# Kernel optimization log

Hardware: AMD Instinct MI355X
Metric: run time of the kernel (lower is better)

Reference implementation:

```python
import jax, jax.numpy as jnp
import numpy as np
from jax import lax

WIN = 11  # window_size


def _uniform_filter_valid(x, win):
    """Separable uniform (box) filter, VALID padding. x: [B,1,H,W].
    Equivalent to scipy uniform_filter followed by skimage's pad-cropping,
    since cropped positions only use fully-interior windows."""
    kh = jnp.full((1, 1, win, 1), 1.0 / win, dtype=x.dtype)
    kw = jnp.full((1, 1, 1, win), 1.0 / win, dtype=x.dtype)
    dn = ('NCHW', 'OIHW', 'NCHW')
    x = lax.conv_general_dilated(x, kh, (1, 1), 'VALID', dimension_numbers=dn)
    x = lax.conv_general_dilated(x, kw, (1, 1), 'VALID', dimension_numbers=dn)
    return x


def _ssim_loss(pred, target, win):
    # skimage structural_similarity with gaussian_weights=False, data_range=1.0
    data_range = 1.0
    C1 = (0.01 * data_range) ** 2
    C2 = (0.03 * data_range) ** 2
    NP = win * win
    cov_norm = NP / (NP - 1.0)  # sample covariance correction

    uf = lambda z: _uniform_filter_valid(z, win)
    ux = uf(pred)
    uy = uf(target)
    uxx = uf(pred * pred)
    uyy = uf(target * target)
    uxy = uf(pred * target)

    vx = cov_norm * (uxx - ux * ux)
    vy = cov_norm * (uyy - uy * uy)
    vxy = cov_norm * (uxy - ux * uy)

    A1 = 2.0 * ux * uy + C1
    A2 = 2.0 * vxy + C2
    B1 = ux * ux + uy * uy + C1
    B2 = vx + vy + C2
    S = (A1 * A2) / (B1 * B2)

    # mean SSIM per image, then mean over batch (identical to flat mean here)
    return 1.0 - jnp.mean(S)


def setup_inputs() -> dict:
    key = jax.random.key(0)
    k1, k2 = jax.random.split(key)
    B, C, H, W = 32, 1, 512, 512
    pred = jax.random.uniform(k1, (B, C, H, W), dtype=jnp.float32)
    target = jax.random.uniform(k2, (B, C, H, W), dtype=jnp.float32)
    return {"pred": pred, "target": target}


def reference(pred, target):
    return _ssim_loss(pred, target, WIN)
```

## Files before the change

kernel.cpp:

```cpp
#include <hip/hip_runtime.h>


#define WW 512
#define OH 502
#define BANDR 26
#define NBANDS 20
#define INV_N (1.0f / 8064128.0f)

#define DPP_ADD(x, ctrl, rmask)                                            \
    x += __int_as_float(__builtin_amdgcn_update_dpp(                       \
        0, __float_as_int(x), (ctrl), (rmask), 0xf, true))

__device__ __forceinline__ float wave_iscan(float x) {
    DPP_ADD(x, 0x111, 0xf);
    DPP_ADD(x, 0x112, 0xf);
    DPP_ADD(x, 0x114, 0xf);
    DPP_ADD(x, 0x118, 0xf);
    DPP_ADD(x, 0x142, 0xa);
    DPP_ADD(x, 0x143, 0xc);
    return x;
}

__device__ __forceinline__ float2 hwin(float v0, float v1, int lane) {
    float e = v0 + v1;
    float S = wave_iscan(e);
    float A4 = __shfl(S, lane + 4);
    float A5 = __shfl(S, lane + 5);
    float v5 = __shfl(v0, lane + 5);
    float W0 = A4 - S + e + v5;
    float W1 = A5 - S + v1;
    return make_float2(W0, W1);
}

__device__ __forceinline__ float ssim_term(float s0, float s1, float sq, float sx) {
    const float NP  = 121.f;
    const float cn  = 121.f / 120.f;
    const float C1n = 1e-4f * 121.f * 121.f;
    const float C2n = 9e-4f * 121.f * 121.f;
    float m1 = s0 * s1;
    float q1 = fmaf(s0, s0, s1 * s1);
    float A1 = fmaf(2.f, m1, C1n);
    float B1 = q1 + C1n;
    float A2 = fmaf(2.f * cn, fmaf(NP, sx, -m1), C2n);
    float B2 = fmaf(cn, fmaf(NP, sq, -q1), C2n);
    return A1 * A2 * __builtin_amdgcn_rcpf(B1 * B2);
}

__global__ __launch_bounds__(256)
void ssim_main(const float* __restrict__ Pg, const float* __restrict__ Tg,
               float* __restrict__ outp) {
    const int tid  = threadIdx.x;
    const int lane = tid & 63;
    const int wv   = tid >> 6;
    const int Wid  = blockIdx.x * 4 + wv;
    const int img   = Wid / 100;
    const int rem   = Wid - img * 100;
    const int strip = rem / NBANDS;
    const int band  = rem - strip * NBANDS;

    const int col0 = (strip == 4) ? 472 : strip * 118;
    const int outw = (strip == 4) ? 30 : 118;
    const int y0   = band * BANDR;
    const int rows = min(BANDR, OH - y0);

    const int cload = min(col0 + 2 * lane, 510);
    const bool ok   = lane < (outw >> 1);

    const float* Pb = Pg + img * (WW * WW);
    const float* Tb = Tg + img * (WW * WW);

    float2 prr[11], trr[11];
    float sp0 = 0.f, sp1 = 0.f, st0 = 0.f, st1 = 0.f;
    float sq0 = 0.f, sq1 = 0.f, sx0 = 0.f, sx1 = 0.f;

    #pragma unroll
    for (int r = 0; r < 10; ++r) {
        float2 p = *(const float2*)(Pb + (y0 + r) * WW + cload);
        float2 t = *(const float2*)(Tb + (y0 + r) * WW + cload);
        prr[r] = p; trr[r] = t;
        sp0 += p.x; sp1 += p.y; st0 += t.x; st1 += t.y;
        sq0 = fmaf(p.x, p.x, sq0); sq0 = fmaf(t.x, t.x, sq0);
        sq1 = fmaf(p.y, p.y, sq1); sq1 = fmaf(t.y, t.y, sq1);
        sx0 = fmaf(p.x, t.x, sx0); sx1 = fmaf(p.y, t.y, sx1);
    }
    float2 Pn0 = *(const float2*)(Pb + (y0 + 10) * WW + cload);
    float2 Tn0 = *(const float2*)(Tb + (y0 + 10) * WW + cload);
    float2 Pn1 = *(const float2*)(Pb + (y0 + 11) * WW + cload);
    float2 Tn1 = *(const float2*)(Tb + (y0 + 11) * WW + cload);

    float acc = 0.f;

    for (int yy = 0; yy < rows; yy += 11) {
        #pragma unroll
        for (int j = 0; j < 11; ++j) {
            if (yy + j < rows) {
                const int sn = (10 + j) % 11;
                float2 Pc = Pn0, Tc = Tn0;
                prr[sn] = Pc; trr[sn] = Tc;
                sp0 += Pc.x; sp1 += Pc.y; st0 += Tc.x; st1 += Tc.y;
                sq0 = fmaf(Pc.x, Pc.x, sq0); sq0 = fmaf(Tc.x, Tc.x, sq0);
                sq1 = fmaf(Pc.y, Pc.y, sq1); sq1 = fmaf(Tc.y, Tc.y, sq1);
                sx0 = fmaf(Pc.x, Tc.x, sx0); sx1 = fmaf(Pc.y, Tc.y, sx1);
                Pn0 = Pn1; Tn0 = Tn1;
                int nr = min(y0 + 12 + yy + j, 511);
                Pn1 = *(const float2*)(Pb + nr * WW + cload);
                Tn1 = *(const float2*)(Tb + nr * WW + cload);
                float2 w0 = hwin(sp0, sp1, lane);
                float2 w1 = hwin(st0, st1, lane);
                float2 w2 = hwin(sq0, sq1, lane);
                float2 w3 = hwin(sx0, sx1, lane);
                if (ok) {
                    acc += ssim_term(w0.x, w1.x, w2.x, w3.x);
                    acc += ssim_term(w0.y, w1.y, w2.y, w3.y);
                }
                float2 po = prr[j], to = trr[j];
                sp0 -= po.x; sp1 -= po.y; st0 -= to.x; st1 -= to.y;
                sq0 = fmaf(po.x, -po.x, sq0); sq0 = fmaf(to.x, -to.x, sq0);
                sq1 = fmaf(po.y, -po.y, sq1); sq1 = fmaf(to.y, -to.y, sq1);
                sx0 = fmaf(po.x, -to.x, sx0); sx1 = fmaf(po.y, -to.y, sx1);
            }
        }
    }

    #pragma unroll
    for (int off = 32; off > 0; off >>= 1) acc += __shfl_down(acc, off);
    __shared__ float wred[4];
    if (lane == 0) wred[wv] = acc;
    __syncthreads();
    if (tid == 0) {
        float s = wred[0] + wred[1] + wred[2] + wred[3];
        float contrib = -s * INV_N;
        if (blockIdx.x == 0) contrib += 1.0f;
        atomicAdd(outp, contrib);
    }
}

extern "C" void kernel_launch(void* const* d_in, const int* in_sizes, int n_in,
                              void* d_out, int out_size, void* d_ws, size_t ws_size,
                              hipStream_t stream) {
    const float* pred = (const float*)d_in[0];
    const float* targ = (const float*)d_in[1];
    float* out = (float*)d_out;

    hipMemsetAsync(out, 0, sizeof(float), stream);
    ssim_main<<<dim3(800), dim3(256), 0, stream>>>(pred, targ, out);
}
```

Measured before the change: 112.4 us.

## Use 22-row bands with fixed trip count, deeper prefetch, and packed float2 math

Rows per band drop from 26 to 22 so every band is exactly two 11-row blocks. This removes the per-row bounds check, and only the last band keeps clamping through a TAIL template specialization. The grid grows from 800 to 920 blocks, the load prefetch deepens from two rows to three, and the SSIM arithmetic is rewritten in float2 form so the compiler can use packed FP32 instructions. More bands means more redundant 10-row halo loads per output row, traded for simpler control flow and better latency hiding.

```diff
diff --git a/kernel.cpp b/kernel.cpp
--- a/kernel.cpp
+++ b/kernel.cpp
@@ -3,8 +3,8 @@
 
 #define WW 512
 #define OH 502
-#define BANDR 26
-#define NBANDS 20
+#define BANDR 22
+#define NBANDS 23
 #define INV_N (1.0f / 8064128.0f)
 
 #define DPP_ADD(x, ctrl, rmask)                                            \
@@ -32,18 +32,89 @@
     return make_float2(W0, W1);
 }
 
-__device__ __forceinline__ float ssim_term(float s0, float s1, float sq, float sx) {
-    const float NP  = 121.f;
-    const float cn  = 121.f / 120.f;
-    const float C1n = 1e-4f * 121.f * 121.f;
-    const float C2n = 9e-4f * 121.f * 121.f;
-    float m1 = s0 * s1;
-    float q1 = fmaf(s0, s0, s1 * s1);
-    float A1 = fmaf(2.f, m1, C1n);
-    float B1 = q1 + C1n;
-    float A2 = fmaf(2.f * cn, fmaf(NP, sx, -m1), C2n);
-    float B2 = fmaf(cn, fmaf(NP, sq, -q1), C2n);
-    return A1 * A2 * __builtin_amdgcn_rcpf(B1 * B2);
+__device__ __forceinline__ float2 f2add(float2 a, float2 b){ return make_float2(a.x+b.x, a.y+b.y); }
+__device__ __forceinline__ float2 f2sub(float2 a, float2 b){ return make_float2(a.x-b.x, a.y-b.y); }
+__device__ __forceinline__ float2 f2mul(float2 a, float2 b){ return make_float2(a.x*b.x, a.y*b.y); }
+__device__ __forceinline__ float2 f2fma(float2 a, float2 b, float2 c){
+    return make_float2(fmaf(a.x,b.x,c.x), fmaf(a.y,b.y,c.y)); }
+__device__ __forceinline__ float2 f2fms(float2 a, float2 b, float2 c){
+    return make_float2(fmaf(a.x,b.x,-c.x), fmaf(a.y,b.y,-c.y)); }
+__device__ __forceinline__ float2 f2nfma(float2 a, float2 b, float2 c){
+    return make_float2(fmaf(-a.x,b.x,c.x), fmaf(-a.y,b.y,c.y)); }
+
+__device__ __forceinline__ float ssim2(float2 w0, float2 w1, float2 w2, float2 w3,
+                                       bool valid) {
+    const float NP = 121.f, cn = 121.f/120.f;
+    const float2 C1n = make_float2(1e-4f*121.f*121.f, 1e-4f*121.f*121.f);
+    const float2 C2n = make_float2(9e-4f*121.f*121.f, 9e-4f*121.f*121.f);
+    const float2 NP2 = make_float2(NP, NP);
+    float2 m1 = f2mul(w0, w1);
+    float2 q1 = f2fma(w0, w0, f2mul(w1, w1));
+    float2 A1 = f2fma(make_float2(2.f,2.f), m1, C1n);
+    float2 B1 = f2add(q1, C1n);
+    float2 A2 = f2fma(make_float2(2.f*cn,2.f*cn), f2fms(NP2, w3, m1), C2n);
+    float2 B2 = f2fma(make_float2(cn,cn), f2fms(NP2, w2, q1), C2n);
+    float2 num = f2mul(A1, A2), den = f2mul(B1, B2);
+    float r = fmaf(num.x, __builtin_amdgcn_rcpf(den.x),
+                   num.y * __builtin_amdgcn_rcpf(den.y));
+    return valid ? r : 0.f;
+}
+
+template<bool TAIL>
+__device__ __forceinline__ float run_band(const float* __restrict__ Pc0,
+                                          const float* __restrict__ Tc0,
+                                          int y0, int lane, bool ok) {
+    float2 prr[11], trr[11];
+    float2 sp = make_float2(0,0), st = make_float2(0,0);
+    float2 sq = make_float2(0,0), sx = make_float2(0,0);
+
+    #pragma unroll
+    for (int r = 0; r < 10; ++r) {
+        float2 p = *(const float2*)(Pc0 + (y0 + r) * WW);
+        float2 t = *(const float2*)(Tc0 + (y0 + r) * WW);
+        prr[r] = p; trr[r] = t;
+        sp = f2add(sp, p); st = f2add(st, t);
+        sq = f2fma(p, p, sq); sq = f2fma(t, t, sq);
+        sx = f2fma(p, t, sx);
+    }
+    float2 Pn0 = *(const float2*)(Pc0 + (y0 + 10) * WW);
+    float2 Tn0 = *(const float2*)(Tc0 + (y0 + 10) * WW);
+    float2 Pn1 = *(const float2*)(Pc0 + (y0 + 11) * WW);
+    float2 Tn1 = *(const float2*)(Tc0 + (y0 + 11) * WW);
+    float2 Pn2 = *(const float2*)(Pc0 + (y0 + 12) * WW);
+    float2 Tn2 = *(const float2*)(Tc0 + (y0 + 12) * WW);
+
+    float acc = 0.f;
+
+    #pragma unroll 1
+    for (int blk = 0; blk < 2; ++blk) {
+        #pragma unroll
+        for (int j = 0; j < 11; ++j) {
+            const int sn = (10 + j) % 11;
+            const int y  = y0 + 11 * blk + j;
+            float2 Pc = Pn0, Tc = Tn0;
+            Pn0 = Pn1; Tn0 = Tn1;
+            Pn1 = Pn2; Tn1 = Tn2;
+            const int nr = TAIL ? min(y + 13, 511) : (y + 13);
+            Pn2 = *(const float2*)(Pc0 + nr * WW);
+            Tn2 = *(const float2*)(Tc0 + nr * WW);
+            prr[sn] = Pc; trr[sn] = Tc;
+            sp = f2add(sp, Pc); st = f2add(st, Tc);
+            sq = f2fma(Pc, Pc, sq); sq = f2fma(Tc, Tc, sq);
+            sx = f2fma(Pc, Tc, sx);
+            float2 w0 = hwin(sp.x, sp.y, lane);
+            float2 w1 = hwin(st.x, st.y, lane);
+            float2 w2 = hwin(sq.x, sq.y, lane);
+            float2 w3 = hwin(sx.x, sx.y, lane);
+            const bool valid = ok && (!TAIL || y < OH);
+            acc += ssim2(w0, w1, w2, w3, valid);
+            float2 po = prr[j], to = trr[j];
+            sp = f2sub(sp, po); st = f2sub(st, to);
+            sq = f2nfma(po, po, sq); sq = f2nfma(to, to, sq);
+            sx = f2nfma(po, to, sx);
+        }
+    }
+    return acc;
 }
 
 __global__ __launch_bounds__(256)
@@ -53,74 +124,26 @@
     const int lane = tid & 63;
     const int wv   = tid >> 6;
     const int Wid  = blockIdx.x * 4 + wv;
-    const int img   = Wid / 100;
-    const int rem   = Wid - img * 100;
+    const int img   = Wid / 115;
+    const int rem   = Wid - img * 115;
     const int strip = rem / NBANDS;
     const int band  = rem - strip * NBANDS;
 
     const int col0 = (strip == 4) ? 472 : strip * 118;
     const int outw = (strip == 4) ? 30 : 118;
     const int y0   = band * BANDR;
-    const int rows = min(BANDR, OH - y0);
 
     const int cload = min(col0 + 2 * lane, 510);
     const bool ok   = lane < (outw >> 1);
 
-    const float* Pb = Pg + img * (WW * WW);
-    const float* Tb = Tg + img * (WW * WW);
+    const float* Pc0 = Pg + img * (WW * WW) + cload;
+    const float* Tc0 = Tg + img * (WW * WW) + cload;
 
-    float2 prr[11], trr[11];
-    float sp0 = 0.f, sp1 = 0.f, st0 = 0.f, st1 = 0.f;
-    float sq0 = 0.f, sq1 = 0.f, sx0 = 0.f, sx1 = 0.f;
-
-    #pragma unroll
-    for (int r = 0; r < 10; ++r) {
-        float2 p = *(const float2*)(Pb + (y0 + r) * WW + cload);
-        float2 t = *(const float2*)(Tb + (y0 + r) * WW + cload);
-        prr[r] = p; trr[r] = t;
-        sp0 += p.x; sp1 += p.y; st0 += t.x; st1 += t.y;
-        sq0 = fmaf(p.x, p.x, sq0); sq0 = fmaf(t.x, t.x, sq0);
-        sq1 = fmaf(p.y, p.y, sq1); sq1 = fmaf(t.y, t.y, sq1);
-        sx0 = fmaf(p.x, t.x, sx0); sx1 = fmaf(p.y, t.y, sx1);
-    }
-    float2 Pn0 = *(const float2*)(Pb + (y0 + 10) * WW + cload);
-    float2 Tn0 = *(const float2*)(Tb + (y0 + 10) * WW + cload);
-    float2 Pn1 = *(const float2*)(Pb + (y0 + 11) * WW + cload);
-    float2 Tn1 = *(const float2*)(Tb + (y0 + 11) * WW + cload);
-
-    float acc = 0.f;
-
-    for (int yy = 0; yy < rows; yy += 11) {
-        #pragma unroll
-        for (int j = 0; j < 11; ++j) {
-            if (yy + j < rows) {
-                const int sn = (10 + j) % 11;
-                float2 Pc = Pn0, Tc = Tn0;
-                prr[sn] = Pc; trr[sn] = Tc;
-                sp0 += Pc.x; sp1 += Pc.y; st0 += Tc.x; st1 += Tc.y;
-                sq0 = fmaf(Pc.x, Pc.x, sq0); sq0 = fmaf(Tc.x, Tc.x, sq0);
-                sq1 = fmaf(Pc.y, Pc.y, sq1); sq1 = fmaf(Tc.y, Tc.y, sq1);
-                sx0 = fmaf(Pc.x, Tc.x, sx0); sx1 = fmaf(Pc.y, Tc.y, sx1);
-                Pn0 = Pn1; Tn0 = Tn1;
-                int nr = min(y0 + 12 + yy + j, 511);
-                Pn1 = *(const float2*)(Pb + nr * WW + cload);
-                Tn1 = *(const float2*)(Tb + nr * WW + cload);
-                float2 w0 = hwin(sp0, sp1, lane);
-                float2 w1 = hwin(st0, st1, lane);
-                float2 w2 = hwin(sq0, sq1, lane);
-                float2 w3 = hwin(sx0, sx1, lane);
-                if (ok) {
-                    acc += ssim_term(w0.x, w1.x, w2.x, w3.x);
-                    acc += ssim_term(w0.y, w1.y, w2.y, w3.y);
-                }
-                float2 po = prr[j], to = trr[j];
-                sp0 -= po.x; sp1 -= po.y; st0 -= to.x; st1 -= to.y;
-                sq0 = fmaf(po.x, -po.x, sq0); sq0 = fmaf(to.x, -to.x, sq0);
-                sq1 = fmaf(po.y, -po.y, sq1); sq1 = fmaf(to.y, -to.y, sq1);
-                sx0 = fmaf(po.x, -to.x, sx0); sx1 = fmaf(po.y, -to.y, sx1);
-            }
-        }
-    }
+    float acc;
+    if (band == NBANDS - 1)
+        acc = run_band<true >(Pc0, Tc0, y0, lane, ok);
+    else
+        acc = run_band<false>(Pc0, Tc0, y0, lane, ok);
 
     #pragma unroll
     for (int off = 32; off > 0; off >>= 1) acc += __shfl_down(acc, off);
@@ -143,5 +166,5 @@
     float* out = (float*)d_out;
 
     hipMemsetAsync(out, 0, sizeof(float), stream);
-    ssim_main<<<dim3(800), dim3(256), 0, stream>>>(pred, targ, out);
+    ssim_main<<<dim3(920), dim3(256), 0, stream>>>(pred, targ, out);
 }
```

New measurement: 110.7 us. No clear change (-1.5%).
